# Performance work log

Hardware: AMD Instinct MI355X
Metric: run time of the kernel (lower is better)

## Reference

```python
import jax, jax.numpy as jnp
import numpy as np

TEMPERATURE = 0.1
B, D = 8192, 128
NUM_CLASSES = 100

def setup_inputs() -> dict:
    key = jax.random.key(0)
    k1, k2 = jax.random.split(key)
    embeddings = jax.random.normal(k1, (B, D), dtype=jnp.float32)
    labels = jax.random.randint(k2, (B,), 0, NUM_CLASSES, dtype=jnp.int64)
    return {"embeddings": embeddings, "labels": labels}

def reference(embeddings, labels):
    b = embeddings.shape[0]
    # L2-normalize rows (F.normalize with eps to avoid div-by-zero)
    norm = jnp.maximum(jnp.linalg.norm(embeddings, axis=1, keepdims=True), 1e-12)
    emb = embeddings / norm
    # [B, B] cosine similarities scaled by temperature
    sim = jnp.matmul(emb, emb.T) / TEMPERATURE
    eye = jnp.eye(b, dtype=jnp.float32)
    pos_mask = (labels[:, None] == labels[None, :]).astype(jnp.float32) - eye
    all_mask = 1.0 - eye
    # Original computes exp(sim*mask)*mask; since mask is {0,1}, this equals
    # exp(sim) summed over the masked entries.
    exp_sim = jnp.exp(sim)
    pos_sum = jnp.sum(exp_sim * pos_mask, axis=1)  # sum over positives j != i
    all_sum = jnp.sum(exp_sim * all_mask, axis=1)  # sum over all j != i
    valid = pos_sum > 0.0  # rows with no positives are skipped in the original
    pos_safe = jnp.where(valid, pos_sum, 1.0)
    all_safe = jnp.where(valid, all_sum, 1.0)
    row_loss = -jnp.log(pos_safe / all_safe)
    n_valid = jnp.sum(valid.astype(jnp.float32))
    loss = jnp.sum(jnp.where(valid, row_loss, 0.0)) / jnp.maximum(n_valid, 1.0)
    return loss
```

## Files before the change

kernel.cpp:

```cpp
#include <hip/hip_runtime.h>
#include <hip/hip_bf16.h>


#define B_ROWS 8192
#define D_DIM 128
#define K_SCALE 14.426950408889634f
#define JSPLIT 32
#define JCHUNK (B_ROWS / JSPLIT)
#define TILE_J 64
#define NT (JCHUNK / TILE_J)
#define BM 256

typedef __attribute__((ext_vector_type(8))) short bf16x8;
typedef __attribute__((ext_vector_type(16))) float f32x16;
typedef __attribute__((ext_vector_type(4))) unsigned int u32x4;
typedef unsigned int u32;
typedef unsigned long long u64;

static __device__ __forceinline__ unsigned short bf16_bits(float x) {
  __hip_bfloat16 h = __float2bfloat16(x);
  unsigned short u;
  __builtin_memcpy(&u, &h, 2);
  return u;
}
static __device__ __forceinline__ float f32_from_bits(u32 b) {
  float f;
  __builtin_memcpy(&f, &b, 4);
  return f;
}
static __device__ __forceinline__ float bf16f(unsigned short u) {
  return f32_from_bits((u32)u << 16);
}

__global__ __launch_bounds__(256) void prep_kernel(
    const float* __restrict__ E, const long long* __restrict__ labels,
    __hip_bfloat16* __restrict__ Ebf, int* __restrict__ lab32,
    unsigned char* __restrict__ lab8p, float* __restrict__ diag) {
  const int wid = threadIdx.x >> 6, lane = threadIdx.x & 63;
  const int row = blockIdx.x * 4 + wid;
  const float2 v = *(const float2*)(E + (u64)row * D_DIM + lane * 2);
  float ss = v.x * v.x + v.y * v.y;
#pragma unroll
  for (int m = 1; m < 64; m <<= 1) ss += __shfl_xor(ss, m);
  const float scale = 1.0f / fmaxf(sqrtf(ss), 1e-12f);
  const unsigned short bx = bf16_bits(v.x * scale);
  const unsigned short by = bf16_bits(v.y * scale);
  ((u32*)Ebf)[(u64)row * (D_DIM / 2) + lane] = ((u32)by << 16) | bx;
  const float fx = bf16f(bx), fy = bf16f(by);
  const float ax = bf16f(bf16_bits(fx * K_SCALE));
  const float ay = bf16f(bf16_bits(fy * K_SCALE));
  float dot = ax * fx + ay * fy;
#pragma unroll
  for (int m = 1; m < 64; m <<= 1) dot += __shfl_xor(dot, m);
  if (lane == 0) diag[row] = __builtin_amdgcn_exp2f(dot);

  const int gtid = blockIdx.x * 256 + threadIdx.x;
  if (gtid < B_ROWS) {
    const int lab = (int)labels[gtid];
    lab32[gtid] = lab;
    const int local = gtid & 31;
    const int h = (local >> 2) & 1;
    const int r = (local & 3) + 4 * (local >> 3);
    lab8p[(gtid & ~31) + h * 16 + r] = (unsigned char)lab;
  }
}

__global__ __launch_bounds__(256) void sim_kernel(
    const __hip_bfloat16* __restrict__ Ebf, const int* __restrict__ lab32,
    const unsigned char* __restrict__ lab8p, float* __restrict__ pos_part,
    float* __restrict__ all_part) {
  __shared__ __align__(16) unsigned char lds[2][TILE_J * 256];

  const int t = threadIdx.x;
  const int wid = t >> 6, lane = t & 63;
  const int l31 = lane & 31, hi = lane >> 5;
  const int i0w = blockIdx.x * BM + wid * 64;
  const int jbase0 = blockIdx.y * JCHUNK;

  bf16x8 ifragA[8], ifragB[8];
#pragma unroll
  for (int iset = 0; iset < 2; ++iset) {
    const __hip_bfloat16* src =
        Ebf + (u64)(i0w + iset * 32 + l31) * D_DIM + hi * 8;
#pragma unroll
    for (int ks = 0; ks < 8; ++ks) {
      bf16x8 raw = *(const bf16x8*)(src + ks * 16);
      bf16x8 s;
#pragma unroll
      for (int e = 0; e < 8; ++e)
        s[e] = (short)bf16_bits(bf16f((unsigned short)raw[e]) * K_SCALE);
      if (iset == 0)
        ifragA[ks] = s;
      else
        ifragB[ks] = s;
    }
  }
  const int labi0 = lab32[i0w + l31];
  const int labi1 = lab32[i0w + 32 + l31];

  const u32 key = lane & 15;
  const u32 M = (key & 14) << 4;
  const u32 base2 = (u32)(l31 * 256) + (((hi ^ (key & 1)) & 1) << 4);

  const unsigned char* gsrc[4];
  {
    const unsigned char* gb = (const unsigned char*)Ebf;
    const int l4 = lane >> 4, sl = lane & 15;
#pragma unroll
    for (int i = 0; i < 4; ++i) {
      const int rloc = wid * 16 + i * 4 + l4;
      gsrc[i] =
          gb + (u64)(jbase0 + rloc) * 256 + (u64)((sl ^ (i * 4 + l4)) * 16);
    }
  }

  auto stage = [&](int buf) {
#pragma unroll
    for (int i = 0; i < 4; ++i) {
      __builtin_amdgcn_global_load_lds(
          (const __attribute__((address_space(1))) u32*)(gsrc[i]),
          (__attribute__((address_space(3)))
               u32*)(&lds[buf][wid * 4096 + i * 1024]),
          16, 0, 0);
      gsrc[i] += TILE_J * 256;
    }
  };

  float pos0 = 0.f, pos1 = 0.f, all0 = 0.f, all1 = 0.f;

  stage(0);
  __syncthreads();

  for (int tile = 0; tile < NT; ++tile) {
    const int cur = tile & 1;
    if (tile + 1 < NT) stage(cur ^ 1);
    const int jbase = jbase0 + tile * TILE_J;
    const unsigned char* lbuf = lds[cur];
#pragma unroll
    for (int jsub = 0; jsub < 2; ++jsub) {
      f32x16 acc0 = {}, acc1 = {};
#pragma unroll
      for (int ks = 0; ks < 8; ++ks) {
        bf16x8 jfrag = *(const bf16x8*)(lbuf + base2 +
                                        (((u32)(ks << 5)) ^ M) + jsub * 8192);
        acc0 = __builtin_amdgcn_mfma_f32_32x32x16_bf16(jfrag, ifragA[ks], acc0,
                                                       0, 0, 0);
        acc1 = __builtin_amdgcn_mfma_f32_32x32x16_bf16(jfrag, ifragB[ks], acc1,
                                                       0, 0, 0);
      }
      const u32x4 labv = *(const u32x4*)(lab8p + jbase + jsub * 32 + hi * 16);
#pragma unroll
      for (int r = 0; r < 16; ++r) {
        const int labj = (int)((labv[r >> 2] >> ((r & 3) * 8)) & 0xff);
        const float p0 = __builtin_amdgcn_exp2f(acc0[r]);
        const float p1 = __builtin_amdgcn_exp2f(acc1[r]);
        all0 += p0;
        all1 += p1;
        pos0 += (labj == labi0) ? p0 : 0.f;
        pos1 += (labj == labi1) ? p1 : 0.f;
      }
    }
    __syncthreads();
  }

  pos0 += __shfl_xor(pos0, 32);
  all0 += __shfl_xor(all0, 32);
  pos1 += __shfl_xor(pos1, 32);
  all1 += __shfl_xor(all1, 32);
  if (hi == 0) {
    const u64 off = (u64)blockIdx.y * B_ROWS;
    pos_part[off + i0w + l31] = pos0;
    all_part[off + i0w + l31] = all0;
    pos_part[off + i0w + 32 + l31] = pos1;
    all_part[off + i0w + 32 + l31] = all1;
  }
}

__global__ __launch_bounds__(256) void fin1_kernel(
    const float* __restrict__ pos_part, const float* __restrict__ all_part,
    const float* __restrict__ diag, float* __restrict__ fin_s,
    float* __restrict__ fin_c) {
  const int row = blockIdx.x * 256 + threadIdx.x;
  float ps = 0.f, as_ = 0.f;
#pragma unroll
  for (int js = 0; js < JSPLIT; ++js) {
    ps += pos_part[(u64)js * B_ROWS + row];
    as_ += all_part[(u64)js * B_ROWS + row];
  }
  const float d = diag[row];
  ps -= d;
  as_ -= d;
  float s = 0.f, c = 0.f;
  if (ps > 0.f) {
    s = logf(as_) - logf(ps);
    c = 1.f;
  }
#pragma unroll
  for (int m = 1; m < 64; m <<= 1) {
    s += __shfl_xor(s, m);
    c += __shfl_xor(c, m);
  }
  __shared__ float ls[4], lc[4];
  const int wid = threadIdx.x >> 6, lane = threadIdx.x & 63;
  if (lane == 0) {
    ls[wid] = s;
    lc[wid] = c;
  }
  __syncthreads();
  if (threadIdx.x == 0) {
    fin_s[blockIdx.x] = ls[0] + ls[1] + ls[2] + ls[3];
    fin_c[blockIdx.x] = lc[0] + lc[1] + lc[2] + lc[3];
  }
}

__global__ __launch_bounds__(64) void fin2_kernel(const float* __restrict__
                                                      fin_s,
                                                  const float* __restrict__
                                                      fin_c,
                                                  float* __restrict__ out) {
  const int lane = threadIdx.x;
  float s = (lane < 32) ? fin_s[lane] : 0.f;
  float c = (lane < 32) ? fin_c[lane] : 0.f;
#pragma unroll
  for (int m = 1; m < 32; m <<= 1) {
    s += __shfl_xor(s, m);
    c += __shfl_xor(c, m);
  }
  if (lane == 0) out[0] = s / fmaxf(c, 1.0f);
}

extern "C" void kernel_launch(void* const* d_in, const int* in_sizes, int n_in,
                              void* d_out, int out_size, void* d_ws,
                              size_t ws_size, hipStream_t stream) {
  const float* E = (const float*)d_in[0];
  const long long* labels = (const long long*)d_in[1];

  float* pos_part = (float*)d_ws;
  float* all_part = pos_part + JSPLIT * B_ROWS;
  int* lab32 = (int*)(all_part + JSPLIT * B_ROWS);
  float* diag = (float*)(lab32 + B_ROWS);
  unsigned char* lab8p = (unsigned char*)(diag + B_ROWS);
  float* fin_s = (float*)(lab8p + B_ROWS);
  float* fin_c = fin_s + 32;
  __hip_bfloat16* Ebf = (__hip_bfloat16*)(fin_c + 32);

  prep_kernel<<<B_ROWS / 4, 256, 0, stream>>>(E, labels, Ebf, lab32, lab8p,
                                              diag);
  sim_kernel<<<dim3(B_ROWS / BM, JSPLIT), 256, 0, stream>>>(
      Ebf, lab32, lab8p, pos_part, all_part);
  fin1_kernel<<<B_ROWS / 256, 256, 0, stream>>>(pos_part, all_part, diag,
                                                fin_s, fin_c);
  fin2_kernel<<<1, 64, 0, stream>>>(fin_s, fin_c, (float*)d_out);
}
```

Baseline: 45.64 us.

## Precompute scaled bf16 embeddings in prep and fuse final reductions via ticket

The prep kernel now also writes a second bf16 copy of the normalized embeddings pre-multiplied by the log2e/temperature scale, so the sim kernel loads its i-fragments directly instead of rescaling and rounding them per block. The two finalisation kernels are merged into one, using an atomic ticket so the last block does the global sum, which saves a kernel launch. The sim kernel also gets a launch-bounds occupancy hint of 3 blocks. In exchange, prep writes an extra 2 MB array, and the finalisation depends on the ticket being reset inside prep.

```diff
diff --git a/kernel.cpp b/kernel.cpp
--- a/kernel.cpp
+++ b/kernel.cpp
@@ -34,8 +34,10 @@
 
 __global__ __launch_bounds__(256) void prep_kernel(
     const float* __restrict__ E, const long long* __restrict__ labels,
-    __hip_bfloat16* __restrict__ Ebf, int* __restrict__ lab32,
-    unsigned char* __restrict__ lab8p, float* __restrict__ diag) {
+    __hip_bfloat16* __restrict__ Ebf, __hip_bfloat16* __restrict__ Ebf2,
+    int* __restrict__ lab32, unsigned char* __restrict__ lab8p,
+    float* __restrict__ diag, u32* __restrict__ ticket) {
+  if (blockIdx.x == 0 && threadIdx.x == 0) *ticket = 0u;
   const int wid = threadIdx.x >> 6, lane = threadIdx.x & 63;
   const int row = blockIdx.x * 4 + wid;
   const float2 v = *(const float2*)(E + (u64)row * D_DIM + lane * 2);
@@ -47,9 +49,10 @@
   const unsigned short by = bf16_bits(v.y * scale);
   ((u32*)Ebf)[(u64)row * (D_DIM / 2) + lane] = ((u32)by << 16) | bx;
   const float fx = bf16f(bx), fy = bf16f(by);
-  const float ax = bf16f(bf16_bits(fx * K_SCALE));
-  const float ay = bf16f(bf16_bits(fy * K_SCALE));
-  float dot = ax * fx + ay * fy;
+  const unsigned short axb = bf16_bits(fx * K_SCALE);
+  const unsigned short ayb = bf16_bits(fy * K_SCALE);
+  ((u32*)Ebf2)[(u64)row * (D_DIM / 2) + lane] = ((u32)ayb << 16) | axb;
+  float dot = bf16f(axb) * fx + bf16f(ayb) * fy;
 #pragma unroll
   for (int m = 1; m < 64; m <<= 1) dot += __shfl_xor(dot, m);
   if (lane == 0) diag[row] = __builtin_amdgcn_exp2f(dot);
@@ -65,8 +68,9 @@
   }
 }
 
-__global__ __launch_bounds__(256) void sim_kernel(
-    const __hip_bfloat16* __restrict__ Ebf, const int* __restrict__ lab32,
+__global__ __launch_bounds__(256, 3) void sim_kernel(
+    const __hip_bfloat16* __restrict__ Ebf,
+    const __hip_bfloat16* __restrict__ Ebf2, const int* __restrict__ lab32,
     const unsigned char* __restrict__ lab8p, float* __restrict__ pos_part,
     float* __restrict__ all_part) {
   __shared__ __align__(16) unsigned char lds[2][TILE_J * 256];
@@ -78,21 +82,13 @@
   const int jbase0 = blockIdx.y * JCHUNK;
 
   bf16x8 ifragA[8], ifragB[8];
-#pragma unroll
-  for (int iset = 0; iset < 2; ++iset) {
-    const __hip_bfloat16* src =
-        Ebf + (u64)(i0w + iset * 32 + l31) * D_DIM + hi * 8;
+  {
+    const __hip_bfloat16* srcA = Ebf2 + (u64)(i0w + l31) * D_DIM + hi * 8;
+    const __hip_bfloat16* srcB = srcA + 32 * D_DIM;
 #pragma unroll
     for (int ks = 0; ks < 8; ++ks) {
-      bf16x8 raw = *(const bf16x8*)(src + ks * 16);
-      bf16x8 s;
-#pragma unroll
-      for (int e = 0; e < 8; ++e)
-        s[e] = (short)bf16_bits(bf16f((unsigned short)raw[e]) * K_SCALE);
-      if (iset == 0)
-        ifragA[ks] = s;
-      else
-        ifragB[ks] = s;
+      ifragA[ks] = *(const bf16x8*)(srcA + ks * 16);
+      ifragB[ks] = *(const bf16x8*)(srcB + ks * 16);
     }
   }
   const int labi0 = lab32[i0w + l31];
@@ -176,10 +172,11 @@
   }
 }
 
-__global__ __launch_bounds__(256) void fin1_kernel(
+__global__ __launch_bounds__(256) void fin_kernel(
     const float* __restrict__ pos_part, const float* __restrict__ all_part,
     const float* __restrict__ diag, float* __restrict__ fin_s,
-    float* __restrict__ fin_c) {
+    float* __restrict__ fin_c, u32* __restrict__ ticket,
+    float* __restrict__ out) {
   const int row = blockIdx.x * 256 + threadIdx.x;
   float ps = 0.f, as_ = 0.f;
 #pragma unroll
@@ -208,25 +205,23 @@
   }
   __syncthreads();
   if (threadIdx.x == 0) {
-    fin_s[blockIdx.x] = ls[0] + ls[1] + ls[2] + ls[3];
-    fin_c[blockIdx.x] = lc[0] + lc[1] + lc[2] + lc[3];
-  }
-}
-
-__global__ __launch_bounds__(64) void fin2_kernel(const float* __restrict__
-                                                      fin_s,
-                                                  const float* __restrict__
-                                                      fin_c,
-                                                  float* __restrict__ out) {
-  const int lane = threadIdx.x;
-  float s = (lane < 32) ? fin_s[lane] : 0.f;
-  float c = (lane < 32) ? fin_c[lane] : 0.f;
-#pragma unroll
-  for (int m = 1; m < 32; m <<= 1) {
-    s += __shfl_xor(s, m);
-    c += __shfl_xor(c, m);
-  }
-  if (lane == 0) out[0] = s / fmaxf(c, 1.0f);
+    __hip_atomic_store(&fin_s[blockIdx.x], ls[0] + ls[1] + ls[2] + ls[3],
+                       __ATOMIC_RELEASE, __HIP_MEMORY_SCOPE_AGENT);
+    __hip_atomic_store(&fin_c[blockIdx.x], lc[0] + lc[1] + lc[2] + lc[3],
+                       __ATOMIC_RELEASE, __HIP_MEMORY_SCOPE_AGENT);
+    const u32 tk = __hip_atomic_fetch_add(ticket, 1u, __ATOMIC_ACQ_REL,
+                                          __HIP_MEMORY_SCOPE_AGENT);
+    if (tk == 31u) {
+      float ts = 0.f, tc = 0.f;
+      for (int b = 0; b < 32; ++b) {
+        ts += __hip_atomic_load(&fin_s[b], __ATOMIC_ACQUIRE,
+                                __HIP_MEMORY_SCOPE_AGENT);
+        tc += __hip_atomic_load(&fin_c[b], __ATOMIC_ACQUIRE,
+                                __HIP_MEMORY_SCOPE_AGENT);
+      }
+      out[0] = ts / fmaxf(tc, 1.0f);
+    }
+  }
 }
 
 extern "C" void kernel_launch(void* const* d_in, const int* in_sizes, int n_in,
@@ -242,13 +237,14 @@
   unsigned char* lab8p = (unsigned char*)(diag + B_ROWS);
   float* fin_s = (float*)(lab8p + B_ROWS);
   float* fin_c = fin_s + 32;
-  __hip_bfloat16* Ebf = (__hip_bfloat16*)(fin_c + 32);
-
-  prep_kernel<<<B_ROWS / 4, 256, 0, stream>>>(E, labels, Ebf, lab32, lab8p,
-                                              diag);
+  u32* ticket = (u32*)(fin_c + 32);
+  __hip_bfloat16* Ebf = (__hip_bfloat16*)(ticket + 4);
+  __hip_bfloat16* Ebf2 = Ebf + (u64)B_ROWS * D_DIM;
+
+  prep_kernel<<<B_ROWS / 4, 256, 0, stream>>>(E, labels, Ebf, Ebf2, lab32,
+                                              lab8p, diag, ticket);
   sim_kernel<<<dim3(B_ROWS / BM, JSPLIT), 256, 0, stream>>>(
-      Ebf, lab32, lab8p, pos_part, all_part);
-  fin1_kernel<<<B_ROWS / 256, 256, 0, stream>>>(pos_part, all_part, diag,
-                                                fin_s, fin_c);
-  fin2_kernel<<<1, 64, 0, stream>>>(fin_s, fin_c, (float*)d_out);
-}
+      Ebf, Ebf2, lab32, lab8p, pos_part, all_part);
+  fin_kernel<<<JSPLIT, 256, 0, stream>>>(pos_part, all_part, diag, fin_s,
+                                         fin_c, ticket, (float*)d_out);
+}
```

Result: slower. 53.28 us (+16.7%).
